# Performance work log

Measured on AMD Instinct MI355X. Metric: run time of the kernel, lower is better.

## Reference

```python
import jax, jax.numpy as jnp
import numpy as np

N = 50000
IN_DIM = 256
HID = 64
HEADS = 4
OUT_DIM = 40
E = 800000
NEG_SLOPE = 0.2


def setup_inputs() -> dict:
    key = jax.random.key(0)
    ks = jax.random.split(key, 12)
    x = jax.random.normal(ks[0], (N, IN_DIM), dtype=jnp.float32)
    edge_index = jax.random.randint(ks[1], (2, E), 0, N, dtype=jnp.int64)
    s = 0.05
    W1 = jax.random.normal(ks[2], (IN_DIM, HEADS * HID), dtype=jnp.float32) * s
    att_src1 = jax.random.normal(ks[3], (HEADS, HID), dtype=jnp.float32) * s
    att_dst1 = jax.random.normal(ks[4], (HEADS, HID), dtype=jnp.float32) * s
    b1 = jnp.zeros((HEADS * HID,), dtype=jnp.float32)
    W2 = jax.random.normal(ks[5], (HEADS * HID, OUT_DIM), dtype=jnp.float32) * s
    att_src2 = jax.random.normal(ks[6], (1, OUT_DIM), dtype=jnp.float32) * s
    att_dst2 = jax.random.normal(ks[7], (1, OUT_DIM), dtype=jnp.float32) * s
    b2 = jnp.zeros((OUT_DIM,), dtype=jnp.float32)
    return {"x": x, "edge_index": edge_index, "W1": W1, "att_src1": att_src1,
            "att_dst1": att_dst1, "b1": b1, "W2": W2, "att_src2": att_src2,
            "att_dst2": att_dst2, "b2": b2}


def _gat_conv(x, src, dst, W, a_src, a_dst, b, heads, out_ch, concat):
    n = x.shape[0]
    h = (x @ W).reshape(n, heads, out_ch)              # [N,H,C]
    alpha_s = jnp.einsum('nhc,hc->nh', h, a_src)       # [N,H]
    alpha_d = jnp.einsum('nhc,hc->nh', h, a_dst)
    e = jax.nn.leaky_relu(alpha_s[src] + alpha_d[dst], NEG_SLOPE)  # [E,H]
    # segment softmax over destination neighborhoods
    m = jax.ops.segment_max(e, dst, num_segments=n)    # [N,H]
    ex = jnp.exp(e - m[dst])
    denom = jax.ops.segment_sum(ex, dst, num_segments=n)
    alpha = ex / (denom[dst] + 1e-16)                  # [E,H]
    out = jax.ops.segment_sum(h[src] * alpha[:, :, None], dst, num_segments=n)  # [N,H,C]
    out = out.reshape(n, heads * out_ch) if concat else out.mean(axis=1)
    return out + b


def reference(x, edge_index, W1, att_src1, att_dst1, b1, W2, att_src2, att_dst2, b2):
    # PyG GATConv adds self-loops by default
    loops = jnp.arange(N, dtype=edge_index.dtype)
    src = jnp.concatenate([edge_index[0], loops])
    dst = jnp.concatenate([edge_index[1], loops])
    h = _gat_conv(x, src, dst, W1, att_src1, att_dst1, b1, HEADS, HID, True)
    h = jax.nn.elu(h)
    h = _gat_conv(h, src, dst, W2, att_src2, att_dst2, b2, 1, OUT_DIM, False)
    return jax.nn.log_softmax(h, axis=1)
```

## Files before the change

### kernel.cpp

```cpp
#include <hip/hip_runtime.h>
#include <hip/hip_bf16.h>
#include <math.h>

#define NNODES 50000
#define M_PAD  50048
#define IN_DIM 256
#define HID 64
#define HEADS 4
#define OUT_DIM 40
#define NEDGES 800000
#define ETOT (NEDGES + NNODES)
#define NEG_SLOPE 0.2f
#define MAXDEG 64

typedef __attribute__((ext_vector_type(8))) short bf16x8;
typedef __attribute__((ext_vector_type(4))) float f32x4;
typedef __attribute__((ext_vector_type(2))) float f32x2;
typedef unsigned char uchar;

__device__ __forceinline__ ushort f2bf(float f) {
    uint u = __float_as_uint(f);
    u += 0x7FFF + ((u >> 16) & 1);
    return (ushort)(u >> 16);
}
__device__ __forceinline__ uint fkey(float f) {
    uint u = __float_as_uint(f);
    return (u & 0x80000000u) ? ~u : (u | 0x80000000u);
}
__device__ __forceinline__ float fdec(uint k) {
    return (k & 0x80000000u) ? __uint_as_float(k & 0x7fffffffu) : __uint_as_float(~k);
}
__device__ __forceinline__ float wave_reduce_max(float v) {
    #pragma unroll
    for (int off = 32; off > 0; off >>= 1) v = fmaxf(v, __shfl_xor(v, off));
    return v;
}
__device__ __forceinline__ float wave_reduce_sum(float v) {
    #pragma unroll
    for (int off = 32; off > 0; off >>= 1) v += __shfl_xor(v, off);
    return v;
}
__device__ __forceinline__ uchar f2fp8(float v) {
    return (uchar)(__builtin_amdgcn_cvt_pk_fp8_f32(v, v, 0, false) & 0xFF);
}
__device__ __forceinline__ void accum8f8(f32x2* acc2, uint2 hv, float wgt) {
    f32x2 wv = {wgt, wgt};
    f32x2 p;
    p = __builtin_amdgcn_cvt_pk_f32_fp8(hv.x, false); acc2[0] += p * wv;
    p = __builtin_amdgcn_cvt_pk_f32_fp8(hv.x, true);  acc2[1] += p * wv;
    p = __builtin_amdgcn_cvt_pk_f32_fp8(hv.y, false); acc2[2] += p * wv;
    p = __builtin_amdgcn_cvt_pk_f32_fp8(hv.y, true);  acc2[3] += p * wv;
}
__device__ __forceinline__ float lrw(float e, float mm) {
    return __expf(fmaxf(e, NEG_SLOPE * e) - mm);
}

__global__ void prep_kernel(const float* __restrict__ W1, const float* __restrict__ W2,
                            const float* __restrict__ a2s, const float* __restrict__ a2d,
                            const int* __restrict__ ei,
                            ushort* __restrict__ W1t, ushort* __restrict__ W2tb,
                            float* __restrict__ wa_s, float* __restrict__ wa_d,
                            int* __restrict__ counts, int* __restrict__ col) {
    int b = blockIdx.x, t = threadIdx.x;
    if (b < 256) {
        W1t[b * 256 + t] = f2bf(W1[t * 256 + b]);
    } else if (b < 306) {
        int idx = (b - 256) * 256 + t;
        if (idx < 48 * 264) {
            int n = idx / 264, k = idx % 264;
            W2tb[idx] = (n < OUT_DIM && k < 256) ? f2bf(W2[k * OUT_DIM + n]) : (ushort)0;
        }
    } else if (b == 306) {
        float ss = 0.f, sd = 0.f;
        #pragma unroll 8
        for (int c = 0; c < OUT_DIM; c++) {
            float wv = W2[t * OUT_DIM + c];
            ss += wv * a2s[c];
            sd += wv * a2d[c];
        }
        wa_s[t] = ss;
        wa_d[t] = sd;
    } else {
        int idx = (b - 307) * 256 + t;
        if (idx < ETOT) {
            int s, d;
            if (idx < NEDGES) { s = ei[idx]; d = ei[NEDGES + idx]; }
            else { s = idx - NEDGES; d = s; }
            int pos = atomicAdd(&counts[d], 1);
            if (pos < MAXDEG) col[d * MAXDEG + pos] = s;
        }
    }
}

__global__ __launch_bounds__(256) void gemm1_fused(const float* __restrict__ x,
                                                   const ushort* __restrict__ W1t,
                                                   const float* __restrict__ asrc,
                                                   const float* __restrict__ adst,
                                                   uchar* __restrict__ h1f8,
                                                   float* __restrict__ as1,
                                                   float* __restrict__ ad1,
                                                   uint* __restrict__ gb) {
    __shared__ ushort As[64 * 32];
    __shared__ ushort Bs[256 * 32];
    __shared__ uint smax[4];
    int t = threadIdx.x;
    int l = t & 63, wn = t >> 6;
    int m0 = blockIdx.x * 64;
    int lrow = l & 15, lks = l >> 4;
    int ks = lks ^ ((lrow >> 1) & 3);

    f32x4 acc[4][4];
    #pragma unroll
    for (int i = 0; i < 4; i++)
        #pragma unroll
        for (int j = 0; j < 4; j++) acc[i][j] = (f32x4){0.f, 0.f, 0.f, 0.f};

    for (int k0 = 0; k0 < 256; k0 += 32) {
        #pragma unroll
        for (int i = 0; i < 2; i++) {
            int idx = t + 256 * i;
            int row = idx >> 3, c4 = idx & 7;
            int grow = m0 + row;
            float4 v = make_float4(0.f, 0.f, 0.f, 0.f);
            if (grow < NNODES) v = *reinterpret_cast<const float4*>(x + (size_t)grow * 256 + k0 + c4 * 4);
            uint2 p;
            p.x = (uint)f2bf(v.x) | ((uint)f2bf(v.y) << 16);
            p.y = (uint)f2bf(v.z) | ((uint)f2bf(v.w) << 16);
            int slot = (c4 >> 1) ^ ((row >> 1) & 3);
            *reinterpret_cast<uint2*>(&As[row * 32 + slot * 8 + (c4 & 1) * 4]) = p;
        }
        #pragma unroll
        for (int i = 0; i < 4; i++) {
            int idx = t + 256 * i;
            int row = idx >> 2, skb = idx & 3;
            uint4 bv = *reinterpret_cast<const uint4*>(W1t + (size_t)row * 256 + k0 + skb * 8);
            int slot = skb ^ ((row >> 1) & 3);
            *reinterpret_cast<uint4*>(&Bs[row * 32 + slot * 8]) = bv;
        }
        __syncthreads();
        bf16x8 a_frag[4], b_frag[4];
        #pragma unroll
        for (int mf = 0; mf < 4; mf++)
            a_frag[mf] = *reinterpret_cast<const bf16x8*>(&As[(mf * 16 + lrow) * 32 + ks * 8]);
        #pragma unroll
        for (int nf = 0; nf < 4; nf++)
            b_frag[nf] = *reinterpret_cast<const bf16x8*>(&Bs[(wn * 64 + nf * 16 + lrow) * 32 + ks * 8]);
        #pragma unroll
        for (int mf = 0; mf < 4; mf++)
            #pragma unroll
            for (int nf = 0; nf < 4; nf++)
                acc[mf][nf] = __builtin_amdgcn_mfma_f32_16x16x32_bf16(a_frag[mf], b_frag[nf], acc[mf][nf], 0, 0, 0);
        __syncthreads();
    }

    #pragma unroll
    for (int mf = 0; mf < 4; mf++)
        #pragma unroll
        for (int nf = 0; nf < 4; nf++) {
            int col = wn * 64 + nf * 16 + lrow;
            #pragma unroll
            for (int r = 0; r < 4; r++) {
                int row = m0 + mf * 16 + lks * 4 + r;
                h1f8[(size_t)row * 256 + col] = f2fp8(acc[mf][nf][r]);
            }
        }

    float a_s[4], a_d[4];
    #pragma unroll
    for (int nf = 0; nf < 4; nf++) {
        a_s[nf] = asrc[wn * 64 + nf * 16 + lrow];
        a_d[nf] = adst[wn * 64 + nf * 16 + lrow];
    }
    float ps[4][4], pd[4][4];
    #pragma unroll
    for (int mf = 0; mf < 4; mf++)
        #pragma unroll
        for (int r = 0; r < 4; r++) {
            float s = 0.f, d = 0.f;
            #pragma unroll
            for (int nf = 0; nf < 4; nf++) {
                s += acc[mf][nf][r] * a_s[nf];
                d += acc[mf][nf][r] * a_d[nf];
            }
            ps[mf][r] = s; pd[mf][r] = d;
        }
    #pragma unroll
    for (int off = 1; off < 16; off <<= 1)
        #pragma unroll
        for (int mf = 0; mf < 4; mf++)
            #pragma unroll
            for (int r = 0; r < 4; r++) {
                ps[mf][r] += __shfl_xor(ps[mf][r], off);
                pd[mf][r] += __shfl_xor(pd[mf][r], off);
            }
    if (lrow == 0) {
        #pragma unroll
        for (int mf = 0; mf < 4; mf++)
            #pragma unroll
            for (int r = 0; r < 4; r++) {
                int row = m0 + mf * 16 + lks * 4 + r;
                if (row < NNODES) {
                    as1[row * 4 + wn] = ps[mf][r];
                    ad1[row * 4 + wn] = pd[mf][r];
                }
            }
    }
    float vmax = -INFINITY;
    #pragma unroll
    for (int mf = 0; mf < 4; mf++)
        #pragma unroll
        for (int r = 0; r < 4; r++) {
            int row = m0 + mf * 16 + lks * 4 + r;
            if (row < NNODES) vmax = fmaxf(vmax, ps[mf][r]);
        }
    vmax = fmaxf(vmax, __shfl_xor(vmax, 16));
    vmax = fmaxf(vmax, __shfl_xor(vmax, 32));
    if (l == 0) smax[wn] = fkey(vmax);
    __syncthreads();
    if (t < 4) atomicMax(&gb[t], smax[t]);
}

__global__ __launch_bounds__(256) void agg1_kernel(const uchar* __restrict__ h1f8,
                                                   const float* __restrict__ as1,
                                                   const float* __restrict__ ad1,
                                                   const int* __restrict__ cnt,
                                                   const int* __restrict__ col,
                                                   const float* __restrict__ b1,
                                                   const uint* __restrict__ gb,
                                                   const float* __restrict__ wa_s,
                                                   const float* __restrict__ wa_d,
                                                   ushort* __restrict__ out1b,
                                                   float* __restrict__ as2,
                                                   float* __restrict__ ad2) {
    int tid = threadIdx.x;
    int lane = tid & 63, wid = tid >> 6;
    int n = blockIdx.x * 4 + wid;
    int j = lane & 31, half = lane >> 5;
    int myh = j >> 3, sub = j & 3;
    int bcast = lane & ~3;
    int deg = min(cnt[n], MAXDEG);
    const int* cp = col + n * MAXDEG;

    float adn = ad1[n * 4 + myh];
    float g = fdec(gb[myh]);
    float mt = g + adn;
    float mm = fmaxf(mt, NEG_SLOPE * mt);

    f32x2 acc2[4];
    #pragma unroll
    for (int k = 0; k < 4; k++) acc2[k] = (f32x2){0.f, 0.f};
    float ls = 0.f;
    uint jb = (uint)(j * 8);

    for (int done = 0; done < deg; done += 8) {
        int base = done + half * 4;
        int4 ca = *reinterpret_cast<const int4*>(cp + base);
        int s0 = (base + 0 < deg) ? ca.x : 0;
        int s1 = (base + 1 < deg) ? ca.y : 0;
        int s2 = (base + 2 < deg) ? ca.z : 0;
        int s3 = (base + 3 < deg) ? ca.w : 0;
        int sown = sub == 0 ? s0 : sub == 1 ? s1 : sub == 2 ? s2 : s3;
        float q = as1[(uint)(sown * 4 + myh)];
        uint2 h0 = *reinterpret_cast<const uint2*>(h1f8 + (((uint)s0 << 8) + jb));
        uint2 h1v = *reinterpret_cast<const uint2*>(h1f8 + (((uint)s1 << 8) + jb));
        uint2 h2v = *reinterpret_cast<const uint2*>(h1f8 + (((uint)s2 << 8) + jb));
        uint2 h3v = *reinterpret_cast<const uint2*>(h1f8 + (((uint)s3 << 8) + jb));
        float wown = (base + sub < deg) ? lrw(q + adn, mm) : 0.f;
        float w0 = __shfl(wown, bcast + 0);
        float w1 = __shfl(wown, bcast + 1);
        float w2 = __shfl(wown, bcast + 2);
        float w3 = __shfl(wown, bcast + 3);
        ls += (w0 + w1) + (w2 + w3);
        accum8f8(acc2, h0, w0);
        accum8f8(acc2, h1v, w1);
        accum8f8(acc2, h2v, w2);
        accum8f8(acc2, h3v, w3);
    }
    #pragma unroll
    for (int k = 0; k < 4; k++) {
        acc2[k].x += __shfl_xor(acc2[k].x, 32);
        acc2[k].y += __shfl_xor(acc2[k].y, 32);
    }
    ls += __shfl_xor(ls, 32);

    float dinv = 1.f / (ls + 1e-16f);
    float4 bA = *reinterpret_cast<const float4*>(b1 + j * 8);
    float4 bB = *reinterpret_cast<const float4*>(b1 + j * 8 + 4);
    float4 wsA = *reinterpret_cast<const float4*>(wa_s + j * 8);
    float4 wsB = *reinterpret_cast<const float4*>(wa_s + j * 8 + 4);
    float4 wdA = *reinterpret_cast<const float4*>(wa_d + j * 8);
    float4 wdB = *reinterpret_cast<const float4*>(wa_d + j * 8 + 4);
    float o[8];
    o[0] = acc2[0].x * dinv + bA.x; o[1] = acc2[0].y * dinv + bA.y;
    o[2] = acc2[1].x * dinv + bA.z; o[3] = acc2[1].y * dinv + bA.w;
    o[4] = acc2[2].x * dinv + bB.x; o[5] = acc2[2].y * dinv + bB.y;
    o[6] = acc2[3].x * dinv + bB.z; o[7] = acc2[3].y * dinv + bB.w;
    #pragma unroll
    for (int e8 = 0; e8 < 8; e8++) o[e8] = o[e8] > 0.f ? o[e8] : expm1f(o[e8]);
    float dps = o[0] * wsA.x + o[1] * wsA.y + o[2] * wsA.z + o[3] * wsA.w
              + o[4] * wsB.x + o[5] * wsB.y + o[6] * wsB.z + o[7] * wsB.w;
    float dpd = o[0] * wdA.x + o[1] * wdA.y + o[2] * wdA.z + o[3] * wdA.w
              + o[4] * wdB.x + o[5] * wdB.y + o[6] * wdB.z + o[7] * wdB.w;
    #pragma unroll
    for (int off = 1; off < 32; off <<= 1) {
        dps += __shfl_xor(dps, off);
        dpd += __shfl_xor(dpd, off);
    }
    if (lane == 0) { as2[n] = dps; ad2[n] = dpd; }
    if (lane < 32) {
        uint4 pk;
        pk.x = (uint)f2bf(o[0]) | ((uint)f2bf(o[1]) << 16);
        pk.y = (uint)f2bf(o[2]) | ((uint)f2bf(o[3]) << 16);
        pk.z = (uint)f2bf(o[4]) | ((uint)f2bf(o[5]) << 16);
        pk.w = (uint)f2bf(o[6]) | ((uint)f2bf(o[7]) << 16);
        *reinterpret_cast<uint4*>(out1b + ((uint)n * 256 + (uint)j * 8)) = pk;
    }
}

__global__ __launch_bounds__(256) void gemm2_kernel(const ushort* __restrict__ Ag,
                                                    const ushort* __restrict__ Bg,
                                                    const float* __restrict__ as2,
                                                    ushort* __restrict__ h2b,
                                                    uint* __restrict__ gb) {
    __shared__ ushort Bs[48 * 264];
    int t = threadIdx.x;
    int l = t & 63, w = t >> 6;
    int lrow = l & 15, lks = l >> 4;
    for (int idx = t; idx < 48 * 264 / 8; idx += 256)
        reinterpret_cast<uint4*>(Bs)[idx] = reinterpret_cast<const uint4*>(Bg)[idx];
    __syncthreads();

    int m0 = blockIdx.x * 64 + w * 16;
    f32x4 acc[3];
    #pragma unroll
    for (int nf = 0; nf < 3; nf++) acc[nf] = (f32x4){0.f, 0.f, 0.f, 0.f};

    #pragma unroll
    for (int k0 = 0; k0 < 256; k0 += 32) {
        bf16x8 af = *reinterpret_cast<const bf16x8*>(Ag + (size_t)(m0 + lrow) * 256 + k0 + lks * 8);
        #pragma unroll
        for (int nf = 0; nf < 3; nf++) {
            bf16x8 bf = *reinterpret_cast<const bf16x8*>(&Bs[(nf * 16 + lrow) * 264 + k0 + lks * 8]);
            acc[nf] = __builtin_amdgcn_mfma_f32_16x16x32_bf16(af, bf, acc[nf], 0, 0, 0);
        }
    }
    #pragma unroll
    for (int nf = 0; nf < 3; nf++) {
        int c = nf * 16 + lrow;
        if (c < OUT_DIM) {
            #pragma unroll
            for (int r = 0; r < 4; r++) {
                int row = m0 + lks * 4 + r;
                if (row < NNODES) h2b[(size_t)row * OUT_DIM + c] = f2bf(acc[nf][r]);
            }
        }
    }
    if (t < 64) {
        int row = blockIdx.x * 64 + t;
        float v = (row < NNODES) ? as2[row] : -INFINITY;
        v = wave_reduce_max(v);
        if (t == 0) atomicMax(&gb[4], fkey(v));
    }
}

__global__ __launch_bounds__(256) void agg2_kernel(const ushort* __restrict__ h2b,
                                                   const float* __restrict__ as2,
                                                   const float* __restrict__ ad2,
                                                   const int* __restrict__ cnt,
                                                   const int* __restrict__ col,
                                                   const float* __restrict__ b2,
                                                   const uint* __restrict__ gb,
                                                   float* __restrict__ out) {
    int tid = threadIdx.x;
    int lane = tid & 63, wid = tid >> 6;
    int n = blockIdx.x * 4 + wid;
    int j = lane & 31, half = lane >> 5;
    int sub = j & 3;
    int bcast = lane & ~3;
    int deg = min(cnt[n], MAXDEG);
    const int* cp = col + n * MAXDEG;
    float adn = ad2[n];
    float g = fdec(gb[4]);
    float mt = g + adn;
    float mm = fmaxf(mt, NEG_SLOPE * mt);

    bool act = j < 20;
    uint jo = (uint)(j * 2);
    f32x2 a2 = {0.f, 0.f};
    float ls = 0.f;

    for (int done = 0; done < deg; done += 8) {
        int base = done + half * 4;
        int4 ca = *reinterpret_cast<const int4*>(cp + base);
        int s0 = (base + 0 < deg) ? ca.x : 0;
        int s1 = (base + 1 < deg) ? ca.y : 0;
        int s2 = (base + 2 < deg) ? ca.z : 0;
        int s3 = (base + 3 < deg) ? ca.w : 0;
        int sown = sub == 0 ? s0 : sub == 1 ? s1 : sub == 2 ? s2 : s3;
        float q = as2[(uint)sown];
        uint v0 = 0, v1 = 0, v2 = 0, v3 = 0;
        if (act) {
            v0 = *reinterpret_cast<const uint*>(h2b + ((uint)s0 * 40 + jo));
            v1 = *reinterpret_cast<const uint*>(h2b + ((uint)s1 * 40 + jo));
            v2 = *reinterpret_cast<const uint*>(h2b + ((uint)s2 * 40 + jo));
            v3 = *reinterpret_cast<const uint*>(h2b + ((uint)s3 * 40 + jo));
        }
        float wown = (base + sub < deg) ? lrw(q + adn, mm) : 0.f;
        float w0 = __shfl(wown, bcast + 0);
        float w1 = __shfl(wown, bcast + 1);
        float w2 = __shfl(wown, bcast + 2);
        float w3 = __shfl(wown, bcast + 3);
        ls += (w0 + w1) + (w2 + w3);
        f32x2 hv;
        hv.x = __uint_as_float(v0 << 16); hv.y = __uint_as_float(v0 & 0xFFFF0000u);
        a2 += hv * (f32x2){w0, w0};
        hv.x = __uint_as_float(v1 << 16); hv.y = __uint_as_float(v1 & 0xFFFF0000u);
        a2 += hv * (f32x2){w1, w1};
        hv.x = __uint_as_float(v2 << 16); hv.y = __uint_as_float(v2 & 0xFFFF0000u);
        a2 += hv * (f32x2){w2, w2};
        hv.x = __uint_as_float(v3 << 16); hv.y = __uint_as_float(v3 & 0xFFFF0000u);
        a2 += hv * (f32x2){w3, w3};
    }
    a2.x += __shfl_xor(a2.x, 32);
    a2.y += __shfl_xor(a2.y, 32);
    ls += __shfl_xor(ls, 32);

    bool lead = lane < 20;
    float v0 = -INFINITY, v1 = -INFINITY;
    if (lead) {
        float2 bb = *reinterpret_cast<const float2*>(b2 + 2 * j);
        float dinv = 1.f / (ls + 1e-16f);
        v0 = a2.x * dinv + bb.x;
        v1 = a2.y * dinv + bb.y;
    }
    float mx = wave_reduce_max(fmaxf(v0, v1));
    float es = lead ? (__expf(v0 - mx) + __expf(v1 - mx)) : 0.f;
    float ssum = wave_reduce_sum(es);
    float lg = logf(ssum);
    if (lead) {
        float2 o2 = make_float2(v0 - mx - lg, v1 - mx - lg);
        *reinterpret_cast<float2*>(out + (size_t)n * OUT_DIM + 2 * j) = o2;
    }
}

extern "C" void kernel_launch(void* const* d_in, const int* in_sizes, int n_in,
                              void* d_out, int out_size, void* d_ws, size_t ws_size,
                              hipStream_t stream) {
    const float* x        = (const float*)d_in[0];
    const int*   ei       = (const int*)d_in[1];
    const float* W1       = (const float*)d_in[2];
    const float* att_src1 = (const float*)d_in[3];
    const float* att_dst1 = (const float*)d_in[4];
    const float* b1       = (const float*)d_in[5];
    const float* W2       = (const float*)d_in[6];
    const float* att_src2 = (const float*)d_in[7];
    const float* att_dst2 = (const float*)d_in[8];
    const float* b2       = (const float*)d_in[9];
    float* out = (float*)d_out;

    char* ws = (char*)d_ws;
    auto alloc = [&](size_t bytes) {
        char* p = ws;
        ws += (bytes + 255) & ~(size_t)255;
        return p;
    };
    uchar*  h1f8   = (uchar*)alloc((size_t)M_PAD * 256);
    ushort* out1b  = (ushort*)alloc((size_t)M_PAD * 256 * 2);
    ushort* W1t    = (ushort*)alloc((size_t)256 * 256 * 2);
    ushort* W2tb   = (ushort*)alloc((size_t)48 * 264 * 2);
    ushort* h2b    = (ushort*)alloc((size_t)NNODES * OUT_DIM * 2);
    float*  as1    = (float*)alloc((size_t)NNODES * 4 * 4);
    float*  ad1    = (float*)alloc((size_t)NNODES * 4 * 4);
    float*  as2    = (float*)alloc((size_t)NNODES * 4);
    float*  ad2    = (float*)alloc((size_t)NNODES * 4);
    float*  wa_s   = (float*)alloc((size_t)256 * 4);
    float*  wa_d   = (float*)alloc((size_t)256 * 4);
    int*    counts = (int*)alloc((size_t)(NNODES + 8) * 4);
    uint*   gmaxb  = (uint*)(counts + NNODES);
    int*    col    = (int*)alloc((size_t)NNODES * MAXDEG * 4);
    if ((size_t)(ws - (char*)d_ws) > ws_size) return;

    hipMemsetAsync(counts, 0, (size_t)(NNODES + 8) * 4, stream);

    int prep_blocks = 307 + (ETOT + 255) / 256;
    prep_kernel<<<prep_blocks, 256, 0, stream>>>(W1, W2, att_src2, att_dst2, ei,
                                                 W1t, W2tb, wa_s, wa_d, counts, col);

    gemm1_fused<<<M_PAD / 64, 256, 0, stream>>>(x, W1t, att_src1, att_dst1,
                                                h1f8, as1, ad1, gmaxb);
    agg1_kernel<<<NNODES / 4, 256, 0, stream>>>(h1f8, as1, ad1, counts, col, b1, gmaxb,
                                                wa_s, wa_d, out1b, as2, ad2);
    gemm2_kernel<<<M_PAD / 64, 256, 0, stream>>>(out1b, W2tb, as2, h2b, gmaxb);
    agg2_kernel<<<NNODES / 4, 256, 0, stream>>>(h2b, as2, ad2, counts, col, b2, gmaxb, out);
}
```

Measured before the change: 192.7 us.

## Move edge scatter from prep kernel into GEMM1 launch to overlap work

```diff
diff --git a/kernel.cpp b/kernel.cpp
--- a/kernel.cpp
+++ b/kernel.cpp
@@ -12,6 +12,8 @@
 #define ETOT (NEDGES + NNODES)
 #define NEG_SLOPE 0.2f
 #define MAXDEG 64
+#define SCAT_BLKS ((ETOT + 255) / 256)
+#define GEMM1_BLKS (M_PAD / 64)
 
 typedef __attribute__((ext_vector_type(8))) short bf16x8;
 typedef __attribute__((ext_vector_type(4))) float f32x4;
@@ -55,12 +57,14 @@
     return __expf(fmaxf(e, NEG_SLOPE * e) - mm);
 }
 
-__global__ void prep_kernel(const float* __restrict__ W1, const float* __restrict__ W2,
-                            const float* __restrict__ a2s, const float* __restrict__ a2d,
-                            const int* __restrict__ ei,
-                            ushort* __restrict__ W1t, ushort* __restrict__ W2tb,
-                            float* __restrict__ wa_s, float* __restrict__ wa_d,
-                            int* __restrict__ counts, int* __restrict__ col) {
+__global__ __launch_bounds__(256) void prep1_kernel(const float* __restrict__ W1,
+                                                    const float* __restrict__ W2,
+                                                    const float* __restrict__ a2s,
+                                                    const float* __restrict__ a2d,
+                                                    ushort* __restrict__ W1t,
+                                                    ushort* __restrict__ W2tb,
+                                                    float* __restrict__ wa_s,
+                                                    float* __restrict__ wa_d) {
     int b = blockIdx.x, t = threadIdx.x;
     if (b < 256) {
         W1t[b * 256 + t] = f2bf(W1[t * 256 + b]);
@@ -70,7 +74,7 @@
             int n = idx / 264, k = idx % 264;
             W2tb[idx] = (n < OUT_DIM && k < 256) ? f2bf(W2[k * OUT_DIM + n]) : (ushort)0;
         }
-    } else if (b == 306) {
+    } else {
         float ss = 0.f, sd = 0.f;
         #pragma unroll 8
         for (int c = 0; c < OUT_DIM; c++) {
@@ -80,8 +84,23 @@
         }
         wa_s[t] = ss;
         wa_d[t] = sd;
-    } else {
-        int idx = (b - 307) * 256 + t;
+    }
+}
+
+__global__ __launch_bounds__(256) void gemm1_scatter(const float* __restrict__ x,
+                                                     const ushort* __restrict__ W1t,
+                                                     const float* __restrict__ asrc,
+                                                     const float* __restrict__ adst,
+                                                     const int* __restrict__ ei,
+                                                     uchar* __restrict__ h1f8,
+                                                     float* __restrict__ as1,
+                                                     float* __restrict__ ad1,
+                                                     uint* __restrict__ gb,
+                                                     int* __restrict__ counts,
+                                                     int* __restrict__ col) {
+    int t = threadIdx.x;
+    if (blockIdx.x < SCAT_BLKS) {
+        int idx = blockIdx.x * 256 + t;
         if (idx < ETOT) {
             int s, d;
             if (idx < NEDGES) { s = ei[idx]; d = ei[NEDGES + idx]; }
@@ -89,23 +108,13 @@
             int pos = atomicAdd(&counts[d], 1);
             if (pos < MAXDEG) col[d * MAXDEG + pos] = s;
         }
-    }
-}
-
-__global__ __launch_bounds__(256) void gemm1_fused(const float* __restrict__ x,
-                                                   const ushort* __restrict__ W1t,
-                                                   const float* __restrict__ asrc,
-                                                   const float* __restrict__ adst,
-                                                   uchar* __restrict__ h1f8,
-                                                   float* __restrict__ as1,
-                                                   float* __restrict__ ad1,
-                                                   uint* __restrict__ gb) {
+        return;
+    }
     __shared__ ushort As[64 * 32];
     __shared__ ushort Bs[256 * 32];
     __shared__ uint smax[4];
-    int t = threadIdx.x;
     int l = t & 63, wn = t >> 6;
-    int m0 = blockIdx.x * 64;
+    int m0 = (blockIdx.x - SCAT_BLKS) * 64;
     int lrow = l & 15, lks = l >> 4;
     int ks = lks ^ ((lrow >> 1) & 3);
 
@@ -157,11 +166,11 @@
     for (int mf = 0; mf < 4; mf++)
         #pragma unroll
         for (int nf = 0; nf < 4; nf++) {
-            int col = wn * 64 + nf * 16 + lrow;
+            int col_ = wn * 64 + nf * 16 + lrow;
             #pragma unroll
             for (int r = 0; r < 4; r++) {
                 int row = m0 + mf * 16 + lks * 4 + r;
-                h1f8[(size_t)row * 256 + col] = f2fp8(acc[mf][nf][r]);
+                h1f8[(size_t)row * 256 + col_] = f2fp8(acc[mf][nf][r]);
             }
         }
 
@@ -482,12 +491,12 @@
 
     hipMemsetAsync(counts, 0, (size_t)(NNODES + 8) * 4, stream);
 
-    int prep_blocks = 307 + (ETOT + 255) / 256;
-    prep_kernel<<<prep_blocks, 256, 0, stream>>>(W1, W2, att_src2, att_dst2, ei,
-                                                 W1t, W2tb, wa_s, wa_d, counts, col);
-
-    gemm1_fused<<<M_PAD / 64, 256, 0, stream>>>(x, W1t, att_src1, att_dst1,
-                                                h1f8, as1, ad1, gmaxb);
+    prep1_kernel<<<307, 256, 0, stream>>>(W1, W2, att_src2, att_dst2,
+                                          W1t, W2tb, wa_s, wa_d);
+
+    gemm1_scatter<<<SCAT_BLKS + GEMM1_BLKS, 256, 0, stream>>>(
+        x, W1t, att_src1, att_dst1, ei, h1f8, as1, ad1, gmaxb, counts, col);
+
     agg1_kernel<<<NNODES / 4, 256, 0, stream>>>(h1f8, as1, ad1, counts, col, b1, gmaxb,
                                                 wa_s, wa_d, out1b, as2, ad2);
     gemm2_kernel<<<M_PAD / 64, 256, 0, stream>>>(out1b, W2tb, as2, h2b, gmaxb);
```

After: 202.8 us. 5.2% more time.

## Partition edge scatter by destination range across block groups with vectorized loads

Applied to the files above, without the earlier changes.

```diff
diff --git a/kernel.cpp b/kernel.cpp
--- a/kernel.cpp
+++ b/kernel.cpp
@@ -12,6 +12,8 @@
 #define ETOT (NEDGES + NNODES)
 #define NEG_SLOPE 0.2f
 #define MAXDEG 64
+#define SCAT_CH 416
+#define PREP_BLKS (307 + SCAT_CH * 8)
 
 typedef __attribute__((ext_vector_type(8))) short bf16x8;
 typedef __attribute__((ext_vector_type(4))) float f32x4;
@@ -54,6 +56,9 @@
 __device__ __forceinline__ float lrw(float e, float mm) {
     return __expf(fmaxf(e, NEG_SLOPE * e) - mm);
 }
+__device__ __forceinline__ uint dpart(int d) {
+    return ((uint)d * 10737u) >> 26;
+}
 
 __global__ void prep_kernel(const float* __restrict__ W1, const float* __restrict__ W2,
                             const float* __restrict__ a2s, const float* __restrict__ a2d,
@@ -62,6 +67,40 @@
                             float* __restrict__ wa_s, float* __restrict__ wa_d,
                             int* __restrict__ counts, int* __restrict__ col) {
     int b = blockIdx.x, t = threadIdx.x;
+    if (b >= 307) {
+        int b2 = b - 307;
+        uint part = (uint)(b2 & 7);
+        int chunk = b2 >> 3;
+        int base = chunk * 2048 + t * 8;
+        if (base >= ETOT) return;
+        int s[8], d[8];
+        if (base + 8 <= NEDGES) {
+            int4 sa = *reinterpret_cast<const int4*>(ei + base);
+            int4 sb = *reinterpret_cast<const int4*>(ei + base + 4);
+            int4 da = *reinterpret_cast<const int4*>(ei + NEDGES + base);
+            int4 db = *reinterpret_cast<const int4*>(ei + NEDGES + base + 4);
+            s[0] = sa.x; s[1] = sa.y; s[2] = sa.z; s[3] = sa.w;
+            s[4] = sb.x; s[5] = sb.y; s[6] = sb.z; s[7] = sb.w;
+            d[0] = da.x; d[1] = da.y; d[2] = da.z; d[3] = da.w;
+            d[4] = db.x; d[5] = db.y; d[6] = db.z; d[7] = db.w;
+        } else {
+            #pragma unroll
+            for (int k = 0; k < 8; k++) {
+                int idx = base + k;
+                if (idx < NEDGES) { s[k] = ei[idx]; d[k] = ei[NEDGES + idx]; }
+                else if (idx < ETOT) { s[k] = idx - NEDGES; d[k] = s[k]; }
+                else { s[k] = 0; d[k] = -1; }
+            }
+        }
+        #pragma unroll
+        for (int k = 0; k < 8; k++) {
+            if (d[k] >= 0 && dpart(d[k]) == part) {
+                int pos = atomicAdd(&counts[d[k]], 1);
+                if (pos < MAXDEG) col[d[k] * MAXDEG + pos] = s[k];
+            }
+        }
+        return;
+    }
     if (b < 256) {
         W1t[b * 256 + t] = f2bf(W1[t * 256 + b]);
     } else if (b < 306) {
@@ -70,7 +109,7 @@
             int n = idx / 264, k = idx % 264;
             W2tb[idx] = (n < OUT_DIM && k < 256) ? f2bf(W2[k * OUT_DIM + n]) : (ushort)0;
         }
-    } else if (b == 306) {
+    } else {
         float ss = 0.f, sd = 0.f;
         #pragma unroll 8
         for (int c = 0; c < OUT_DIM; c++) {
@@ -80,15 +119,6 @@
         }
         wa_s[t] = ss;
         wa_d[t] = sd;
-    } else {
-        int idx = (b - 307) * 256 + t;
-        if (idx < ETOT) {
-            int s, d;
-            if (idx < NEDGES) { s = ei[idx]; d = ei[NEDGES + idx]; }
-            else { s = idx - NEDGES; d = s; }
-            int pos = atomicAdd(&counts[d], 1);
-            if (pos < MAXDEG) col[d * MAXDEG + pos] = s;
-        }
     }
 }
 
@@ -157,11 +187,11 @@
     for (int mf = 0; mf < 4; mf++)
         #pragma unroll
         for (int nf = 0; nf < 4; nf++) {
-            int col = wn * 64 + nf * 16 + lrow;
+            int col_ = wn * 64 + nf * 16 + lrow;
             #pragma unroll
             for (int r = 0; r < 4; r++) {
                 int row = m0 + mf * 16 + lks * 4 + r;
-                h1f8[(size_t)row * 256 + col] = f2fp8(acc[mf][nf][r]);
+                h1f8[(size_t)row * 256 + col_] = f2fp8(acc[mf][nf][r]);
             }
         }
 
@@ -482,9 +512,8 @@
 
     hipMemsetAsync(counts, 0, (size_t)(NNODES + 8) * 4, stream);
 
-    int prep_blocks = 307 + (ETOT + 255) / 256;
-    prep_kernel<<<prep_blocks, 256, 0, stream>>>(W1, W2, att_src2, att_dst2, ei,
-                                                 W1t, W2tb, wa_s, wa_d, counts, col);
+    prep_kernel<<<PREP_BLKS, 256, 0, stream>>>(W1, W2, att_src2, att_dst2, ei,
+                                               W1t, W2tb, wa_s, wa_d, counts, col);
 
     gemm1_fused<<<M_PAD / 64, 256, 0, stream>>>(x, W1t, att_src1, att_dst1,
                                                 h1f8, as1, ad1, gmaxb);
```

Result: faster. 180.3 us (-6.4%).
